# Performance work log

Hardware: AMD Instinct MI355X
Metric: run time of the kernel (lower is better)

## Reference

```python
import jax, jax.numpy as jnp
import numpy as np

N = 4096
CIN = 128
COUT = 128
J = 2
DENSITY = 0.01  # ~40 nonzeros per Laplacian row


def _mask(k):
    m = (jax.random.uniform(k, (N, N)) < DENSITY).astype(jnp.float32)
    # Laplacians have nonzero diagonals; also guarantees no empty softmax rows
    return jnp.maximum(m, jnp.eye(N, dtype=jnp.float32))


def setup_inputs() -> dict:
    key = jax.random.key(0)
    ks = jax.random.split(key, 9)
    x = jax.random.normal(ks[0], (N, CIN), dtype=jnp.float32)
    Lup = _mask(ks[1])
    Ldown = _mask(ks[2])
    P = jax.random.normal(ks[3], (N, N), dtype=jnp.float32) / np.float32(np.sqrt(N))
    weight_irr = jax.random.normal(ks[4], (J, CIN, COUT), dtype=jnp.float32) * 0.05
    weight_sol = jax.random.normal(ks[5], (J, CIN, COUT), dtype=jnp.float32) * 0.05
    weight_har = jax.random.normal(ks[6], (CIN, COUT), dtype=jnp.float32) * 0.05
    att_irr = jax.random.normal(ks[7], (2 * J * COUT, 1), dtype=jnp.float32) * 0.05
    att_sol = jax.random.normal(ks[8], (2 * J * COUT, 1), dtype=jnp.float32) * 0.05
    return {"x": x, "Lup": Lup, "Ldown": Ldown, "P": P,
            "weight_irr": weight_irr, "weight_sol": weight_sol,
            "weight_har": weight_har, "att_irr": att_irr, "att_sol": att_sol}


def _masked_row_softmax(e, mask):
    # torch.sparse.softmax over the mask's nonzero pattern, dim=1, then to_dense
    on = mask > 0
    z = jnp.where(on, e, -jnp.inf)
    m = jnp.max(z, axis=1, keepdims=True)
    m = jnp.where(jnp.isfinite(m), m, 0.0)  # guard fully-masked rows
    p = jnp.exp(z - m)                      # exp(-inf)=0 off-pattern
    s = jnp.sum(p, axis=1, keepdims=True)
    s = jnp.where(s == 0, 1.0, s)
    return jnp.where(on, p / s, 0.0)


def _branch(x, weight, att, mask):
    j, cout = weight.shape[0], weight.shape[2]
    att_slice = j * cout
    h = jnp.einsum('ni,jio->jno', x, weight)         # [J, N, Cout]
    hf = h.reshape(-1, att_slice)                    # [N, J*Cout] (row-major, as torch)
    src = hf @ att[:att_slice]                       # [N, 1]
    dst = hf @ att[att_slice:]                       # [N, 1]
    e = jax.nn.leaky_relu(src + dst.T)               # [N, N], slope 0.01 (torch default)
    alpha = _masked_row_softmax(e, mask)             # [N, N]
    powers = [alpha]
    for _ in range(j - 1):
        powers.append(powers[-1] @ alpha)            # iterative matrix powers
    alpha_exp = jnp.stack(powers)                    # [J, N, N]
    # torch.sum with no dim: full reduction to a SCALAR (faithful to source)
    return jnp.sum(jnp.einsum('jnm,jmo->jno', alpha_exp, h))


def reference(x, Lup, Ldown, P, weight_irr, weight_sol, weight_har, att_irr, att_sol):
    z_irr = _branch(x, weight_irr, att_irr, Ldown)   # scalar
    z_sol = _branch(x, weight_sol, att_sol, Lup)     # scalar
    z_har = (P @ x) @ weight_har                     # [N, Cout]
    return z_irr + z_sol + z_har
```

## Files before the change

kernel.cpp:

```cpp
#include <hip/hip_runtime.h>

typedef __attribute__((ext_vector_type(8))) short short8b;
typedef __attribute__((ext_vector_type(4))) float f32x4;

#define NEG_SENTINEL (-1e30f)

constexpr int C_OFF    = 0;
constexpr int C2_OFF   = 8192;
constexpr int SC_OFF   = 16384;
constexpr int FLAG_I   = 16390;
constexpr int ZERO_N   = 16448;
constexpr int V_OFF    = 16448;
constexpr int NP_OFF   = 19008;
constexpr int SRC_OFF  = 100928;
constexpr int RM_OFF   = 117312;
constexpr int RS_OFF   = 125504;
constexpr int NNZ_OFF  = 133696;
constexpr int CCI_OFF  = 141888;
constexpr int XBT_OFF  = 666176;
constexpr int TP_OFF   = 928320;
constexpr int BM_OFF   = 5122624;

__device__ __forceinline__ unsigned short f2bf(float f) {
  unsigned int u = __float_as_uint(f);
  u += 0x7FFFu + ((u >> 16) & 1u);
  return (unsigned short)(u >> 16);
}
__device__ __forceinline__ float bf2f(unsigned short b) {
  return __uint_as_float(((unsigned int)b) << 16);
}
__device__ __forceinline__ float scrub(float v) {
  unsigned int u = __float_as_uint(v);
  return ((u & 0x7F800000u) == 0x7F800000u) ? 0.f : v;
}

__global__ __launch_bounds__(128) void k_vvec(const void* __restrict__ xin,
                                              const void* __restrict__ w_irr,
                                              const void* __restrict__ w_sol,
                                              const void* __restrict__ att_irr,
                                              const void* __restrict__ att_sol,
                                              int* __restrict__ flagp,
                                              float* __restrict__ vvec) {
  __shared__ int sdet[128];
  int t = threadIdx.x;
  unsigned int ef = (((const unsigned int*)xin)[t] >> 7) & 0xFFu;
  sdet[t] = (ef >= 100u && ef <= 150u) ? 1 : 0;
  __syncthreads();
  for (int d = 64; d > 0; d >>= 1) { if (t < d) sdet[t] += sdet[t + d]; __syncthreads(); }
  int f = (sdet[0] >= 96) ? 1 : 0;
  if (blockIdx.x == 0 && t == 0) *flagp = f;
  int bx = blockIdx.x;
  int b = bx / 10, rem = bx % 10, j = rem / 5, tt = rem % 5;
  const void* Wv = (b == 0 ? w_irr : w_sol);
  const void* Av = (b == 0 ? att_irr : att_sol);
  int i = t;
  float s = 0.f;
  if (f) {
    const unsigned short* Wr = (const unsigned short*)Wv + (size_t)j * 16384 + (size_t)i * 128;
    const unsigned short* Ar = (const unsigned short*)Av + tt * 128;
    for (int o = 0; o < 128; o += 8) {
      uint4 wq = *(const uint4*)(Wr + o);
      unsigned int ww[4] = {wq.x, wq.y, wq.z, wq.w};
      float cf[8];
      if (tt < 4) {
        uint4 aq = *(const uint4*)(Ar + o);
        unsigned int aa[4] = {aq.x, aq.y, aq.z, aq.w};
#pragma unroll
        for (int u = 0; u < 4; ++u) {
          cf[2 * u] = bf2f((unsigned short)(aa[u] & 0xFFFFu));
          cf[2 * u + 1] = bf2f((unsigned short)(aa[u] >> 16));
        }
      } else {
#pragma unroll
        for (int e = 0; e < 8; ++e) cf[e] = 1.0f;
      }
#pragma unroll
      for (int u = 0; u < 4; ++u) {
        s += bf2f((unsigned short)(ww[u] & 0xFFFFu)) * cf[2 * u];
        s += bf2f((unsigned short)(ww[u] >> 16)) * cf[2 * u + 1];
      }
    }
  } else {
    const float* Wr = (const float*)Wv + (size_t)j * 16384 + (size_t)i * 128;
    const float* Ar = (const float*)Av + tt * 128;
    for (int o = 0; o < 128; o += 4) {
      float4 wq = *(const float4*)(Wr + o);
      float4 aq = {1.f, 1.f, 1.f, 1.f};
      if (tt < 4) aq = *(const float4*)(Ar + o);
      s += wq.x * aq.x + wq.y * aq.y + wq.z * aq.z + wq.w * aq.w;
    }
  }
  vvec[bx * 128 + i] = s;
}

__global__ __launch_bounds__(256) void k_prep(const void* __restrict__ xin,
                                              const int* __restrict__ flag,
                                              const float* __restrict__ vvec,
                                              unsigned short* __restrict__ xbT,
                                              float* __restrict__ np,
                                              float* __restrict__ srcdst) {
  __shared__ __align__(16) float ldsx[64 * 130];
  __shared__ __align__(16) float ldsv[2560];
  __shared__ float ldsp[4 * 1280];
  __shared__ float npl[1280];
  int f = *flag;
  int t = threadIdx.x, nb = blockIdx.x * 64;
  for (int q = 0; q < 16; ++q) {
    int idx = q * 256 + t;
    int row = idx >> 6, cp = idx & 63;
    float vx, vy;
    if (f) {
      unsigned int u = ((const unsigned int*)xin)[(size_t)(nb + row) * 64 + cp];
      vx = bf2f((unsigned short)(u & 0xFFFFu));
      vy = bf2f((unsigned short)(u >> 16));
    } else {
      float2 v = ((const float2*)xin)[(size_t)(nb + row) * 64 + cp];
      vx = v.x; vy = v.y;
    }
    ldsx[row * 130 + cp * 2] = vx;
    ldsx[row * 130 + cp * 2 + 1] = vy;
  }
  for (int q = 0; q < 10; ++q) { int idx = q * 256 + t; ldsv[idx] = vvec[idx]; }
  __syncthreads();
  for (int q = 0; q < 32; ++q) {
    int idx = q * 256 + t;
    int c = idx >> 6, n = idx & 63;
    xbT[(size_t)c * 4096 + nb + n] = f2bf(ldsx[n * 130 + c]);
  }
  int row = t & 63, qq = t >> 6, i0 = qq * 32;
  float acc[20];
#pragma unroll
  for (int k = 0; k < 20; ++k) acc[k] = 0.f;
  for (int i = i0; i < i0 + 32; i += 2) {
    float2 xv = *(const float2*)&ldsx[row * 130 + i];
#pragma unroll
    for (int k = 0; k < 20; ++k) {
      float2 vk = *(const float2*)&ldsv[k * 128 + i];
      acc[k] += xv.x * vk.x + xv.y * vk.y;
    }
  }
#pragma unroll
  for (int k = 0; k < 20; ++k) ldsp[qq * 1280 + row * 20 + k] = acc[k];
  __syncthreads();
  for (int rep = 0; rep < 5; ++rep) {
    int idx = rep * 256 + t;
    int k = idx >> 6, rr = idx & 63;
    float s = ldsp[rr * 20 + k] + ldsp[1280 + rr * 20 + k] +
              ldsp[2560 + rr * 20 + k] + ldsp[3840 + rr * 20 + k];
    npl[k * 64 + rr] = s;
    np[(size_t)k * 4096 + nb + rr] = s;
  }
  __syncthreads();
  {
    int b = t >> 7, j = (t >> 6) & 1, kind = (t >> 5) & 1, q = t & 31;
    int bl = q * 2;
    int r = j * 2048 + (nb >> 1) + q;
    int kidx = b * 10 + j * 5 + kind * 2;
    float val = npl[kidx * 64 + bl] + npl[(kidx + 1) * 64 + bl + 1];
    srcdst[b * 8192 + kind * 4096 + r] = val;
  }
}

__global__ __launch_bounds__(256) void k_mask(const void* __restrict__ Ldown,
                                              const void* __restrict__ Lup,
                                              const int* __restrict__ flag,
                                              unsigned char* __restrict__ bm) {
  int f = *flag;
  int b = blockIdx.y;
  const void* mask = b ? Lup : Ldown;
  int idx = blockIdx.x * 256 + threadIdx.x;
  unsigned int byte = 0;
  if (f) {
    uint4 v = ((const uint4*)mask)[idx];
    unsigned int wv[4] = {v.x, v.y, v.z, v.w};
#pragma unroll
    for (int u = 0; u < 4; ++u) {
      byte |= ((wv[u] & 0xFFFFu) != 0u ? 1u : 0u) << (2 * u);
      byte |= ((wv[u] >> 16) != 0u ? 1u : 0u) << (2 * u + 1);
    }
  } else {
    const uint4* p = (const uint4*)mask + (size_t)idx * 2;
    uint4 v0 = p[0], v1 = p[1];
    unsigned int wv[8] = {v0.x, v0.y, v0.z, v0.w, v1.x, v1.y, v1.z, v1.w};
#pragma unroll
    for (int u = 0; u < 8; ++u) byte |= (wv[u] != 0u ? 1u : 0u) << u;
  }
  bm[(size_t)b * 2097152 + idx] = (unsigned char)byte;
}

__global__ __launch_bounds__(256) void k_soft(float* __restrict__ ws) {
  const unsigned char* bm = (const unsigned char*)(ws + BM_OFF);
  int b = blockIdx.y, t = threadIdx.x;
  int wid = t >> 6, l = t & 63;
  int r = blockIdx.x * 4 + wid;
  unsigned short* cci = (unsigned short*)(ws + CCI_OFF) + (size_t)(b * 4096 + r) * 128;
  unsigned long long hm =
      ((const unsigned long long*)(bm + ((size_t)b * 4096 + r) * 512))[l];
  int cnt = __popcll(hm);
  int pre = cnt;
  for (int d = 1; d < 64; d <<= 1) {
    int o = __shfl_up(pre, d);
    if (l >= d) pre += o;
  }
  int base = pre - cnt;
  int nz = __shfl(pre, 63);
  if (l == 0) ((int*)ws)[NNZ_OFF + b * 4096 + r] = min(nz, 128);
  const float* srcp = ws + SRC_OFF + b * 8192;
  const float* dstp = srcp + 4096;
  float srcr = srcp[r];
  float ev[6];
  int nh = 0;
  float mx = NEG_SENTINEL, sm = 0.f;
  unsigned long long mm = hm;
  while (mm) {
    int bit = __builtin_ctzll(mm); mm &= mm - 1;
    int m = l * 64 + bit;
    float e = srcr + dstp[m];
    e = (e >= 0.f) ? e : 0.01f * e;
    if (nh < 6) ev[nh] = e;
    ++nh;
    if (e > mx) { sm = sm * __expf(mx - e) + 1.f; mx = e; }
    else        { sm += __expf(e - mx); }
  }
  for (int d = 1; d < 64; d <<= 1) {
    float om = __shfl_xor(mx, d);
    float os = __shfl_xor(sm, d);
    float M = fmaxf(mx, om);
    sm = sm * __expf(mx - M) + os * __expf(om - M);
    mx = M;
  }
  if (l == 0) {
    ws[RM_OFF + b * 4096 + r] = mx;
    ws[RS_OFF + b * 4096 + r] = sm;
  }
  float inv = 1.0f / sm;
  int slot = base, i = 0;
  mm = hm;
  while (mm) {
    int bit = __builtin_ctzll(mm); mm &= mm - 1;
    int m = l * 64 + bit;
    if (slot < 128) cci[slot] = (unsigned short)m;
    ++slot;
    float e;
    if (i < 6) e = ev[i];
    else { e = srcr + dstp[m]; e = (e >= 0.f) ? e : 0.01f * e; }
    ++i;
    atomicAdd(&ws[C_OFF + b * 4096 + m], __expf(e - mx) * inv);
  }
}

__device__ __forceinline__ float alpha_of(const float* ws, int b, int r, int m) {
  const float* srcp = ws + SRC_OFF + b * 8192;
  float e = srcp[r] + srcp[4096 + m];
  e = (e >= 0.f) ? e : 0.01f * e;
  return __expf(e - ws[RM_OFF + b * 4096 + r]) / ws[RS_OFF + b * 4096 + r];
}

__global__ __launch_bounds__(256) void k_c2(float* __restrict__ ws) {
  int b = blockIdx.y;
  int s = blockIdx.x * 256 + threadIdx.x;
  int r = s >> 7, k = s & 127;
  int nz = ((const int*)ws)[NNZ_OFF + b * 4096 + r];
  if (k < nz) {
    int m = ((const unsigned short*)(ws + CCI_OFF))[(size_t)(b * 4096 + r) * 128 + k];
    atomicAdd(&ws[C2_OFF + b * 4096 + m], ws[C_OFF + b * 4096 + r] * alpha_of(ws, b, r, m));
  }
}

__global__ __launch_bounds__(256) void k_scalar(float* __restrict__ ws) {
  int b = blockIdx.x, t = threadIdx.x;
  const float* cb  = ws + C_OFF  + b * 4096;
  const float* c2b = ws + C2_OFF + b * 4096;
  const float* hr0 = ws + NP_OFF + (b * 10 + 4) * 4096;
  const float* hr1 = ws + NP_OFF + (b * 10 + 9) * 4096;
  double acc = 0.0;
  for (int m = t; m < 4096; m += 256)
    acc += (double)scrub(cb[m]) * (double)scrub(hr0[m]) +
           (double)scrub(c2b[m]) * (double)scrub(hr1[m]);
  __shared__ double sd[256];
  sd[t] = acc;
  __syncthreads();
  for (int s = 128; s > 0; s >>= 1) { if (t < s) sd[t] += sd[t + s]; __syncthreads(); }
  if (t == 0) atomicAdd(&ws[SC_OFF], (float)sd[0]);
}

__global__ __launch_bounds__(256) void k_gemm1(const void* __restrict__ P,
                                               const unsigned short* __restrict__ xbT,
                                               const int* __restrict__ flag,
                                               float* __restrict__ TP) {
  __shared__ __align__(16) unsigned short a_lds[64 * 40];
  __shared__ __align__(16) unsigned short b_lds[128 * 40];
  int f = *flag;
  const int mt = blockIdx.x & 63, ks = blockIdx.x >> 6;
  const int mb = mt * 64;
  const int t = threadIdx.x;
  const int w = t >> 6, l = t & 63, quad = l >> 4, lr = l & 15;
  f32x4 acc[8] = {};
  const int arow = t >> 2, akq = (t & 3) << 3;
  const int bn = t >> 1, bh = (t & 1) << 4;
  const int k0 = ks * 512;
  uint4 aU, bU0, bU1;
#define LOADT(IT)                                                              \
  {                                                                            \
    const int kb = k0 + (IT) * 32;                                             \
    if (f) {                                                                   \
      aU = *(const uint4*)((const unsigned short*)P +                          \
                           (size_t)(mb + arow) * 4096 + kb + akq);             \
    } else {                                                                   \
      const float* pa = (const float*)P + (size_t)(mb + arow) * 4096 + kb + akq; \
      float4 f0 = *(const float4*)pa;                                          \
      float4 f1 = *(const float4*)(pa + 4);                                    \
      unsigned short u[8] = {f2bf(f0.x), f2bf(f0.y), f2bf(f0.z), f2bf(f0.w),   \
                             f2bf(f1.x), f2bf(f1.y), f2bf(f1.z), f2bf(f1.w)};  \
      aU = *(const uint4*)u;                                                   \
    }                                                                          \
    const unsigned short* src = xbT + (size_t)bn * 4096 + kb + bh;             \
    bU0 = *(const uint4*)src;                                                  \
    bU1 = *(const uint4*)(src + 8);                                            \
  }
  LOADT(0);
  for (int it = 0; it < 16; ++it) {
    *(uint4*)&a_lds[arow * 40 + akq] = aU;
    *(uint4*)&b_lds[bn * 40 + bh] = bU0;
    *(uint4*)&b_lds[bn * 40 + bh + 8] = bU1;
    __syncthreads();
    if (it < 15) LOADT(it + 1);
    short8b af = *(short8b*)&a_lds[(w * 16 + lr) * 40 + quad * 8];
#pragma unroll
    for (int nt = 0; nt < 8; ++nt) {
      short8b bf = *(short8b*)&b_lds[(nt * 16 + lr) * 40 + quad * 8];
      acc[nt] = __builtin_amdgcn_mfma_f32_16x16x32_bf16(af, bf, acc[nt], 0, 0, 0);
    }
    if (it < 15) __syncthreads();
  }
#undef LOADT
  float* Tp = TP + (size_t)ks * 524288;
#pragma unroll
  for (int nt = 0; nt < 8; ++nt)
#pragma unroll
    for (int rr = 0; rr < 4; ++rr) {
      int row = mb + w * 16 + quad * 4 + rr;
      int col = nt * 16 + lr;
      Tp[(size_t)row * 128 + col] = acc[nt][rr];
    }
}

__global__ __launch_bounds__(256) void k_gemm2(const float* __restrict__ TP,
                                               const void* __restrict__ W,
                                               const float* __restrict__ ws,
                                               void* __restrict__ outv) {
  __shared__ float tl[16 * 128];
  int f = ((const int*)ws)[FLAG_I];
  int t = threadIdx.x;
  int rb = blockIdx.x * 16;
  for (int q = 0; q < 2; ++q) {
    int vi = q * 256 + t;
    size_t base = (size_t)rb * 128 + (size_t)vi * 4;
    float4 s = {0.f, 0.f, 0.f, 0.f};
#pragma unroll
    for (int p = 0; p < 8; ++p) {
      float4 v = *(const float4*)&TP[(size_t)p * 524288 + base];
      s.x += v.x; s.y += v.y; s.z += v.z; s.w += v.w;
    }
    *(float4*)&tl[vi * 4] = s;
  }
  __syncthreads();
  int col = t & 127, rg = t >> 7;
  int r0 = rg * 8;
  float acc[8] = {};
  for (int k = 0; k < 128; k += 4) {
    float w0, w1, w2, w3;
    if (f) {
      const unsigned short* W16 = (const unsigned short*)W;
      w0 = bf2f(W16[(k + 0) * 128 + col]); w1 = bf2f(W16[(k + 1) * 128 + col]);
      w2 = bf2f(W16[(k + 2) * 128 + col]); w3 = bf2f(W16[(k + 3) * 128 + col]);
    } else {
      const float* W32 = (const float*)W;
      w0 = W32[(k + 0) * 128 + col]; w1 = W32[(k + 1) * 128 + col];
      w2 = W32[(k + 2) * 128 + col]; w3 = W32[(k + 3) * 128 + col];
    }
#pragma unroll
    for (int rr = 0; rr < 8; ++rr) {
      float4 tv = *(const float4*)&tl[(r0 + rr) * 128 + k];
      acc[rr] += tv.x * w0 + tv.y * w1 + tv.z * w2 + tv.w * w3;
    }
  }
  float s = scrub(ws[SC_OFF]);
#pragma unroll
  for (int rr = 0; rr < 8; ++rr) {
    size_t oi = (size_t)(rb + r0 + rr) * 128 + col;
    float v = s + acc[rr];
    if (f) ((unsigned short*)outv)[oi] = f2bf(v);
    else   ((float*)outv)[oi] = v;
  }
}

extern "C" void kernel_launch(void* const* d_in, const int* in_sizes, int n_in,
                              void* d_out, int out_size, void* d_ws, size_t ws_size,
                              hipStream_t stream) {
  const void* x       = d_in[0];
  const void* Lup     = d_in[1];
  const void* Ldown   = d_in[2];
  const void* P       = d_in[3];
  const void* w_irr   = d_in[4];
  const void* w_sol   = d_in[5];
  const void* w_har   = d_in[6];
  const void* att_irr = d_in[7];
  const void* att_sol = d_in[8];
  float* ws = (float*)d_ws;

  hipMemsetAsync(d_ws, 0, (size_t)ZERO_N * sizeof(float), stream);
  k_vvec  <<<20, 128, 0, stream>>>(x, w_irr, w_sol, att_irr, att_sol,
                                   (int*)ws + FLAG_I, ws + V_OFF);
  k_prep  <<<64, 256, 0, stream>>>(x, (int*)ws + FLAG_I, ws + V_OFF,
                                   (unsigned short*)(ws + XBT_OFF), ws + NP_OFF,
                                   ws + SRC_OFF);
  k_gemm1 <<<512, 256, 0, stream>>>(P, (const unsigned short*)(ws + XBT_OFF),
                                    (int*)ws + FLAG_I, ws + TP_OFF);
  k_mask  <<<dim3(8192, 2), 256, 0, stream>>>(Ldown, Lup, (int*)ws + FLAG_I,
                                              (unsigned char*)(ws + BM_OFF));
  k_soft  <<<dim3(1024, 2), 256, 0, stream>>>(ws);
  k_c2    <<<dim3(2048, 2), 256, 0, stream>>>(ws);
  k_scalar<<<2, 256, 0, stream>>>(ws);
  k_gemm2 <<<256, 256, 0, stream>>>(ws + TP_OFF, w_har, ws, d_out);
}
```

Before: 322.0 us.

## Coarsen mask bitpacking, drop CSR index buffer, recompute alpha from bitmask in c2

The mask-packing kernel now has each block handle 4096 output bytes. It stages them in shared memory and writes them out as 16-byte vector stores instead of one byte per thread. The softmax kernel no longer builds a per-row column-index list or nnz count. It processes two rows per wave and caches up to 8 values per lane. The second-power kernel walks the bitmask directly and folds c[r]/rowsum into one weight. This is meant to cut the grid sizes, the index-buffer traffic and the narrow stores. The cost is longer serial loops per block and fewer blocks, which may lower occupancy.

```diff
diff --git a/kernel.cpp b/kernel.cpp
--- a/kernel.cpp
+++ b/kernel.cpp
@@ -15,8 +15,6 @@
 constexpr int SRC_OFF  = 100928;
 constexpr int RM_OFF   = 117312;
 constexpr int RS_OFF   = 125504;
-constexpr int NNZ_OFF  = 133696;
-constexpr int CCI_OFF  = 141888;
 constexpr int XBT_OFF  = 666176;
 constexpr int TP_OFF   = 928320;
 constexpr int BM_OFF   = 5122624;
@@ -165,105 +163,129 @@
                                               const void* __restrict__ Lup,
                                               const int* __restrict__ flag,
                                               unsigned char* __restrict__ bm) {
+  __shared__ __align__(16) unsigned char lb[4096];
   int f = *flag;
   int b = blockIdx.y;
   const void* mask = b ? Lup : Ldown;
-  int idx = blockIdx.x * 256 + threadIdx.x;
-  unsigned int byte = 0;
+  int t = threadIdx.x;
+  size_t wg = (size_t)blockIdx.x * 4096;
   if (f) {
-    uint4 v = ((const uint4*)mask)[idx];
-    unsigned int wv[4] = {v.x, v.y, v.z, v.w};
-#pragma unroll
-    for (int u = 0; u < 4; ++u) {
-      byte |= ((wv[u] & 0xFFFFu) != 0u ? 1u : 0u) << (2 * u);
-      byte |= ((wv[u] >> 16) != 0u ? 1u : 0u) << (2 * u + 1);
+    const uint4* in4 = (const uint4*)mask;
+#pragma unroll
+    for (int k = 0; k < 16; ++k) {
+      size_t bi = wg + k * 256 + t;
+      uint4 v = in4[bi];
+      unsigned int by = 0;
+      by |= ((v.x & 0xFFFFu) != 0u ? 1u : 0u) << 0;
+      by |= ((v.x >> 16) != 0u ? 1u : 0u) << 1;
+      by |= ((v.y & 0xFFFFu) != 0u ? 1u : 0u) << 2;
+      by |= ((v.y >> 16) != 0u ? 1u : 0u) << 3;
+      by |= ((v.z & 0xFFFFu) != 0u ? 1u : 0u) << 4;
+      by |= ((v.z >> 16) != 0u ? 1u : 0u) << 5;
+      by |= ((v.w & 0xFFFFu) != 0u ? 1u : 0u) << 6;
+      by |= ((v.w >> 16) != 0u ? 1u : 0u) << 7;
+      lb[k * 256 + t] = (unsigned char)by;
     }
   } else {
-    const uint4* p = (const uint4*)mask + (size_t)idx * 2;
-    uint4 v0 = p[0], v1 = p[1];
-    unsigned int wv[8] = {v0.x, v0.y, v0.z, v0.w, v1.x, v1.y, v1.z, v1.w};
-#pragma unroll
-    for (int u = 0; u < 8; ++u) byte |= (wv[u] != 0u ? 1u : 0u) << u;
-  }
-  bm[(size_t)b * 2097152 + idx] = (unsigned char)byte;
+    const uint4* in4 = (const uint4*)mask;
+#pragma unroll
+    for (int k = 0; k < 16; ++k) {
+      size_t bi = wg + k * 256 + t;
+      uint4 v0 = in4[2 * bi], v1 = in4[2 * bi + 1];
+      unsigned int by = 0;
+      by |= (v0.x != 0u ? 1u : 0u) << 0;
+      by |= (v0.y != 0u ? 1u : 0u) << 1;
+      by |= (v0.z != 0u ? 1u : 0u) << 2;
+      by |= (v0.w != 0u ? 1u : 0u) << 3;
+      by |= (v1.x != 0u ? 1u : 0u) << 4;
+      by |= (v1.y != 0u ? 1u : 0u) << 5;
+      by |= (v1.z != 0u ? 1u : 0u) << 6;
+      by |= (v1.w != 0u ? 1u : 0u) << 7;
+      lb[k * 256 + t] = (unsigned char)by;
+    }
+  }
+  __syncthreads();
+  ((uint4*)(bm + (size_t)b * 2097152 + wg))[t] = ((const uint4*)lb)[t];
 }
 
 __global__ __launch_bounds__(256) void k_soft(float* __restrict__ ws) {
   const unsigned char* bm = (const unsigned char*)(ws + BM_OFF);
   int b = blockIdx.y, t = threadIdx.x;
   int wid = t >> 6, l = t & 63;
-  int r = blockIdx.x * 4 + wid;
-  unsigned short* cci = (unsigned short*)(ws + CCI_OFF) + (size_t)(b * 4096 + r) * 128;
-  unsigned long long hm =
-      ((const unsigned long long*)(bm + ((size_t)b * 4096 + r) * 512))[l];
-  int cnt = __popcll(hm);
-  int pre = cnt;
-  for (int d = 1; d < 64; d <<= 1) {
-    int o = __shfl_up(pre, d);
-    if (l >= d) pre += o;
-  }
-  int base = pre - cnt;
-  int nz = __shfl(pre, 63);
-  if (l == 0) ((int*)ws)[NNZ_OFF + b * 4096 + r] = min(nz, 128);
   const float* srcp = ws + SRC_OFF + b * 8192;
   const float* dstp = srcp + 4096;
-  float srcr = srcp[r];
-  float ev[6];
-  int nh = 0;
-  float mx = NEG_SENTINEL, sm = 0.f;
-  unsigned long long mm = hm;
-  while (mm) {
-    int bit = __builtin_ctzll(mm); mm &= mm - 1;
-    int m = l * 64 + bit;
-    float e = srcr + dstp[m];
-    e = (e >= 0.f) ? e : 0.01f * e;
-    if (nh < 6) ev[nh] = e;
-    ++nh;
-    if (e > mx) { sm = sm * __expf(mx - e) + 1.f; mx = e; }
-    else        { sm += __expf(e - mx); }
-  }
-  for (int d = 1; d < 64; d <<= 1) {
-    float om = __shfl_xor(mx, d);
-    float os = __shfl_xor(sm, d);
-    float M = fmaxf(mx, om);
-    sm = sm * __expf(mx - M) + os * __expf(om - M);
-    mx = M;
-  }
-  if (l == 0) {
-    ws[RM_OFF + b * 4096 + r] = mx;
-    ws[RS_OFF + b * 4096 + r] = sm;
-  }
-  float inv = 1.0f / sm;
-  int slot = base, i = 0;
-  mm = hm;
-  while (mm) {
-    int bit = __builtin_ctzll(mm); mm &= mm - 1;
-    int m = l * 64 + bit;
-    if (slot < 128) cci[slot] = (unsigned short)m;
-    ++slot;
-    float e;
-    if (i < 6) e = ev[i];
-    else { e = srcr + dstp[m]; e = (e >= 0.f) ? e : 0.01f * e; }
-    ++i;
-    atomicAdd(&ws[C_OFF + b * 4096 + m], __expf(e - mx) * inv);
-  }
-}
-
-__device__ __forceinline__ float alpha_of(const float* ws, int b, int r, int m) {
+#pragma unroll
+  for (int rr = 0; rr < 2; ++rr) {
+    int r = blockIdx.x * 8 + wid * 2 + rr;
+    unsigned long long hm =
+        ((const unsigned long long*)(bm + ((size_t)b * 4096 + r) * 512))[l];
+    float srcr = srcp[r];
+    float ev[8];
+    int mv[8];
+    int nh = 0;
+    float mx = NEG_SENTINEL, sm = 0.f;
+    unsigned long long mm = hm;
+    while (mm) {
+      int bit = __builtin_ctzll(mm); mm &= mm - 1;
+      int m = l * 64 + bit;
+      float e = srcr + dstp[m];
+      e = (e >= 0.f) ? e : 0.01f * e;
+      if (nh < 8) { ev[nh] = e; mv[nh] = m; }
+      ++nh;
+      if (e > mx) { sm = sm * __expf(mx - e) + 1.f; mx = e; }
+      else        { sm += __expf(e - mx); }
+    }
+    for (int d = 1; d < 64; d <<= 1) {
+      float om = __shfl_xor(mx, d);
+      float os = __shfl_xor(sm, d);
+      float M = fmaxf(mx, om);
+      sm = sm * __expf(mx - M) + os * __expf(om - M);
+      mx = M;
+    }
+    if (l == 0) {
+      ws[RM_OFF + b * 4096 + r] = mx;
+      ws[RS_OFF + b * 4096 + r] = sm;
+    }
+    float inv = 1.0f / sm;
+    int cap = (nh < 8) ? nh : 8;
+    for (int i = 0; i < cap; ++i)
+      atomicAdd(&ws[C_OFF + b * 4096 + mv[i]], __expf(ev[i] - mx) * inv);
+    if (nh > 8) {
+      int skip = 8;
+      mm = hm;
+      while (mm) {
+        int bit = __builtin_ctzll(mm); mm &= mm - 1;
+        if (skip > 0) { --skip; continue; }
+        int m = l * 64 + bit;
+        float e = srcr + dstp[m];
+        e = (e >= 0.f) ? e : 0.01f * e;
+        atomicAdd(&ws[C_OFF + b * 4096 + m], __expf(e - mx) * inv);
+      }
+    }
+  }
+}
+
+__global__ __launch_bounds__(256) void k_c2(float* __restrict__ ws) {
+  const unsigned char* bm = (const unsigned char*)(ws + BM_OFF);
+  int b = blockIdx.y, t = threadIdx.x;
+  int wid = t >> 6, l = t & 63;
   const float* srcp = ws + SRC_OFF + b * 8192;
-  float e = srcp[r] + srcp[4096 + m];
-  e = (e >= 0.f) ? e : 0.01f * e;
-  return __expf(e - ws[RM_OFF + b * 4096 + r]) / ws[RS_OFF + b * 4096 + r];
-}
-
-__global__ __launch_bounds__(256) void k_c2(float* __restrict__ ws) {
-  int b = blockIdx.y;
-  int s = blockIdx.x * 256 + threadIdx.x;
-  int r = s >> 7, k = s & 127;
-  int nz = ((const int*)ws)[NNZ_OFF + b * 4096 + r];
-  if (k < nz) {
-    int m = ((const unsigned short*)(ws + CCI_OFF))[(size_t)(b * 4096 + r) * 128 + k];
-    atomicAdd(&ws[C2_OFF + b * 4096 + m], ws[C_OFF + b * 4096 + r] * alpha_of(ws, b, r, m));
+  const float* dstp = srcp + 4096;
+#pragma unroll
+  for (int rr = 0; rr < 2; ++rr) {
+    int r = blockIdx.x * 8 + wid * 2 + rr;
+    unsigned long long hm =
+        ((const unsigned long long*)(bm + ((size_t)b * 4096 + r) * 512))[l];
+    float srcr = srcp[r];
+    float rm = ws[RM_OFF + b * 4096 + r];
+    float w = ws[C_OFF + b * 4096 + r] / ws[RS_OFF + b * 4096 + r];
+    while (hm) {
+      int bit = __builtin_ctzll(hm); hm &= hm - 1;
+      int m = l * 64 + bit;
+      float e = srcr + dstp[m];
+      e = (e >= 0.f) ? e : 0.01f * e;
+      atomicAdd(&ws[C2_OFF + b * 4096 + m], __expf(e - rm) * w);
+    }
   }
 }
 
@@ -417,10 +439,10 @@
                                    ws + SRC_OFF);
   k_gemm1 <<<512, 256, 0, stream>>>(P, (const unsigned short*)(ws + XBT_OFF),
                                     (int*)ws + FLAG_I, ws + TP_OFF);
-  k_mask  <<<dim3(8192, 2), 256, 0, stream>>>(Ldown, Lup, (int*)ws + FLAG_I,
-                                              (unsigned char*)(ws + BM_OFF));
-  k_soft  <<<dim3(1024, 2), 256, 0, stream>>>(ws);
-  k_c2    <<<dim3(2048, 2), 256, 0, stream>>>(ws);
+  k_mask  <<<dim3(512, 2), 256, 0, stream>>>(Ldown, Lup, (int*)ws + FLAG_I,
+                                             (unsigned char*)(ws + BM_OFF));
+  k_soft  <<<dim3(512, 2), 256, 0, stream>>>(ws);
+  k_c2    <<<dim3(512, 2), 256, 0, stream>>>(ws);
   k_scalar<<<2, 256, 0, stream>>>(ws);
   k_gemm2 <<<256, 256, 0, stream>>>(ws + TP_OFF, w_har, ws, d_out);
 }
```

After: 320.8 us. Within noise of the previous version (-0.4%).
